# Performance work log

Measured on AMD Instinct MI355X. Metric: run time of the kernel, lower is better.

Reference implementation:

```python
import jax, jax.numpy as jnp
import numpy as np

B, T, D, H = 16, 64, 256, 1536  # batch, num_seq (trg_len), input_dim, hid_dim


def setup_inputs() -> dict:
    key = jax.random.key(0)
    ks = jax.random.split(key, 6)
    def w(k, shape, fan):
        return jax.random.normal(k, shape, jnp.float32) / np.sqrt(fan).astype(np.float32)
    return {
        "batch": jax.random.normal(ks[0], (B, T, D), jnp.float32),
        # PyTorch LSTM params, gate order (i, f, g, o), layer 0 and layer 1
        "W_ih0": w(ks[1], (4 * H, D), H),
        "W_hh0": w(ks[2], (4 * H, H), H),
        "b_ih0": jnp.zeros((4 * H,), jnp.float32),
        "b_hh0": jnp.zeros((4 * H,), jnp.float32),
        "W_ih1": w(ks[3], (4 * H, H), H),
        "W_hh1": w(ks[4], (4 * H, H), H),
        "b_ih1": jnp.zeros((4 * H,), jnp.float32),
        "b_hh1": jnp.zeros((4 * H,), jnp.float32),
    }


def _lstm_cell(pre, c):
    # pre: [4H] pre-activation gates in PyTorch order i, f, g, o
    i, f, g, o = jnp.split(pre, 4, axis=-1)
    c_new = jax.nn.sigmoid(f) * c + jax.nn.sigmoid(i) * jnp.tanh(g)
    h_new = jax.nn.sigmoid(o) * jnp.tanh(c_new)
    return h_new, c_new


def reference(batch, W_ih0, W_hh0, b_ih0, b_hh0, W_ih1, W_hh1, b_ih1, b_hh1):
    hdim = W_hh0.shape[1]
    dt = batch.dtype
    # The original loop runs the unbatched 2-layer LSTM over batch[:, ei, :]
    # (length-B sequence) for ei = 1..T-1, carrying state => one scan over a
    # flattened sequence of length (T-1)*B, ordered ei-major, b-minor.
    seq = batch[:, 1:, :].transpose(1, 0, 2).reshape(-1, batch.shape[2])  # [(T-1)*B, D]
    # Precompute layer-0 input projection as one GEMM (dropout=0.3 is between
    # layers in train mode only; reference is eval mode, so no dropout).
    x_pre0 = seq @ W_ih0.T + (b_ih0 + b_hh0)  # [(T-1)*B, 4H]
    b1 = b_ih1 + b_hh1

    def step(carry, xp0):
        h, c = carry  # each [2, H] (num_layers, hid_dim), unbatched
        h0, c0 = _lstm_cell(xp0 + h[0] @ W_hh0.T, c[0])
        h1, c1 = _lstm_cell(h0 @ W_ih1.T + h[1] @ W_hh1.T + b1, c[1])
        return (jnp.stack([h0, h1]), jnp.stack([c0, c1])), None

    init = (jnp.zeros((2, hdim), dt), jnp.zeros((2, hdim), dt))
    (h_final, c_final), _ = jax.lax.scan(step, init, x_pre0)
    return h_final, c_final  # each [2, H], matching (encoder_hidden, encoder_cell)
```

## Files before the change

### kernel.cpp

```cpp
#include <hip/hip_runtime.h>
#include <cstdint>

#define HDIM   1536
#define DIN    256
#define NSTEP  1008
#define NWG    256
#define TPB    512
#define UPW    6
#define XN     256
#define NREP   8

#define C_H0      0
#define C_H1      1024
#define REP_STRIDE 2048
#define WS_FLAG_W 32768

typedef uint32_t u32x4 __attribute__((ext_vector_type(4)));

__device__ __forceinline__ float bflo(uint32_t p){ union{uint32_t u; float f;} v; v.u = p << 16; return v.f; }
__device__ __forceinline__ float bfhi(uint32_t p){ union{uint32_t u; float f;} v; v.u = p & 0xffff0000u; return v.f; }
__device__ __forceinline__ float bf2f(uint16_t b){ union{uint32_t u; float f;} v; v.u = ((uint32_t)b) << 16; return v.f; }
__device__ __forceinline__ uint16_t f2bf(float f){
    union{float f; uint32_t u;} v; v.f = f;
    uint32_t r = v.u + 0x7fffu + ((v.u >> 16) & 1u);
    return (uint16_t)(r >> 16);
}
__device__ __forceinline__ uint32_t packbf(float lo, float hi){
    return (uint32_t)f2bf(lo) | ((uint32_t)f2bf(hi) << 16);
}
__device__ __forceinline__ float tanh_fast(float x){
    return 1.f - 2.f/(__expf(2.f*x) + 1.f);
}

#if __has_builtin(__builtin_amdgcn_fdot2_f32_bf16)
typedef __bf16 bf16x2 __attribute__((ext_vector_type(2)));
__device__ __forceinline__ float dot2bf(uint32_t a, uint32_t b, float c){
    return __builtin_amdgcn_fdot2_f32_bf16(__builtin_bit_cast(bf16x2, a),
                                           __builtin_bit_cast(bf16x2, b), c, false);
}
#else
__device__ __forceinline__ float dot2bf(uint32_t a, uint32_t b, float c){
    c = fmaf(bflo(a), bflo(b), c);
    c = fmaf(bfhi(a), bfhi(b), c);
    return c;
}
#endif

__device__ __forceinline__ u32x4 poll16(const uint64_t* p){
    u32x4 r;
    asm volatile("global_load_dwordx4 %0, %1, off sc0 sc1\n\t"
                 "s_waitcnt vmcnt(0)"
                 : "=v"(r) : "v"(p) : "memory");
    return r;
}

__device__ __forceinline__ float wave_sum(float x){
    #pragma unroll
    for (int o = 1; o < 64; o <<= 1) x += __shfl_xor(x, o, 64);
    return x;
}

__global__ void init_ws(const uint32_t* __restrict__ w, uint32_t* __restrict__ ws){
    uint64_t* ws64 = (uint64_t*)ws;
    const int i = blockIdx.x * blockDim.x + threadIdx.x;
    if (i < NREP*512){
        const int rep = i >> 9, j = i & 511;
        uint64_t* base = ws64 + rep*REP_STRIDE;
        base[C_H0 + 512 + j] = 0ull;
        base[C_H1 + j]       = 0ull;
        base[C_H1 + 512 + j] = ((uint64_t)1 << 48);
    }
    if (blockIdx.x == 0 && threadIdx.x < 64){
        const int t = threadIdx.x;
        int cnt = 0;
        #pragma unroll
        for (int j = 0; j < 4; ++j){
            const uint32_t v = w[t*4 + j];
            const uint32_t e = (v >> 7) & 0xFFu;
            if (e == 0u || (e >= 0x70u && e <= 0x7Cu)) cnt++;
        }
        #pragma unroll
        for (int o = 1; o < 64; o <<= 1) cnt += __shfl_xor(cnt, o, 64);
        if (t == 0)
            ws[WS_FLAG_W] = (cnt < 128) ? 1u : 0u;
    }
}

__global__ __launch_bounds__(TPB, 2)
void lstm_seq_kernel(const void* __restrict__ batch_,
                     const void* __restrict__ Wih0_,
                     const void* __restrict__ Whh0_,
                     const void* __restrict__ bih0_,
                     const void* __restrict__ bhh0_,
                     const void* __restrict__ Wih1_,
                     const void* __restrict__ Whh1_,
                     const void* __restrict__ bih1_,
                     const void* __restrict__ bhh1_,
                     void* __restrict__ out_,
                     uint32_t* __restrict__ ws)
{
    __shared__ uint32_t lds_w[8*3*8*64];
    __shared__ uint32_t lds_h[1536];
    __shared__ float    lds_pre[48];
    __shared__ float    lds_b[48];
    __shared__ float    lds_c[12];
    __shared__ float    lds_hout[12];

    const int g   = blockIdx.x;
    const int tid = threadIdx.x;
    const int w   = tid >> 6;
    const int l   = tid & 63;

    const uint32_t fp32in = __hip_atomic_load(&ws[WS_FLAG_W],
                             __ATOMIC_RELAXED, __HIP_MEMORY_SCOPE_AGENT);
    uint64_t* ws64 = (uint64_t*)ws;

    if (tid < 24){
        const int uu = tid >> 2, gate = tid & 3;
        const int grow = gate*HDIM + g*UPW + uu;
        if (fp32in){
            lds_b[tid]      = ((const float*)bih0_)[grow] + ((const float*)bhh0_)[grow];
            lds_b[24 + tid] = ((const float*)bih1_)[grow] + ((const float*)bhh1_)[grow];
        } else {
            lds_b[tid]      = bf2f(((const uint16_t*)bih0_)[grow]) + bf2f(((const uint16_t*)bhh0_)[grow]);
            lds_b[24 + tid] = bf2f(((const uint16_t*)bih1_)[grow]) + bf2f(((const uint16_t*)bhh1_)[grow]);
        }
    }
    if (tid < 12){ lds_c[tid] = 0.f; lds_hout[tid] = 0.f; }

    uint32_t w0[3][14];
    uint32_t w1r[3][16];

    if (fp32in){
        const float2* Wih0f = (const float2*)Wih0_;
        const float2* Whh0f = (const float2*)Whh0_;
        const float2* Wih1f = (const float2*)Wih1_;
        const float2* Whh1f = (const float2*)Whh1_;
        #pragma unroll
        for (int j = 0; j < 3; ++j){
            const int rr = w*3 + j;
            const int grow = (rr & 3)*HDIM + g*UPW + (rr >> 2);
            float2 t;
            t = Wih0f[grow*(DIN/2) + l];        w0[j][0] = packbf(t.x, t.y);
            t = Wih0f[grow*(DIN/2) + 64 + l];   w0[j][1] = packbf(t.x, t.y);
            #pragma unroll
            for (int c = 2; c < 14; ++c){
                t = Whh0f[grow*(HDIM/2) + (c-2)*64 + l]; w0[j][c] = packbf(t.x, t.y);
            }
            #pragma unroll
            for (int c = 0; c < 8; ++c){
                t = Wih1f[grow*(HDIM/2) + c*64 + l];
                lds_w[((w*3 + j)*8 + c)*64 + l] = packbf(t.x, t.y);
            }
            #pragma unroll
            for (int c = 8; c < 12; ++c){
                t = Wih1f[grow*(HDIM/2) + c*64 + l]; w1r[j][c-8] = packbf(t.x, t.y);
            }
            #pragma unroll
            for (int c = 12; c < 24; ++c){
                t = Whh1f[grow*(HDIM/2) + (c-12)*64 + l]; w1r[j][c-8] = packbf(t.x, t.y);
            }
        }
    } else {
        const uint32_t* Wih0p = (const uint32_t*)Wih0_;
        const uint32_t* Whh0p = (const uint32_t*)Whh0_;
        const uint32_t* Wih1p = (const uint32_t*)Wih1_;
        const uint32_t* Whh1p = (const uint32_t*)Whh1_;
        #pragma unroll
        for (int j = 0; j < 3; ++j){
            const int rr = w*3 + j;
            const int grow = (rr & 3)*HDIM + g*UPW + (rr >> 2);
            w0[j][0] = Wih0p[grow*(DIN/2) + l];
            w0[j][1] = Wih0p[grow*(DIN/2) + 64 + l];
            #pragma unroll
            for (int c = 2; c < 14; ++c)
                w0[j][c] = Whh0p[grow*(HDIM/2) + (c-2)*64 + l];
            #pragma unroll
            for (int c = 0; c < 8; ++c)
                lds_w[((w*3 + j)*8 + c)*64 + l] = Wih1p[grow*(HDIM/2) + c*64 + l];
            #pragma unroll
            for (int c = 8; c < 12; ++c)
                w1r[j][c-8] = Wih1p[grow*(HDIM/2) + c*64 + l];
            #pragma unroll
            for (int c = 12; c < 24; ++c)
                w1r[j][c-8] = Whh1p[grow*(HDIM/2) + (c-12)*64 + l];
        }
    }

    const int players = tid >> 8;
    const int pidx    = tid & 255;
    uint64_t* myrep   = ws64 + (g & (NREP-1))*REP_STRIDE;

    for (int n = 0; n <= NSTEP; ++n){
        uint32_t xp0, xp1;
        {
            const int nn = (n < NSTEP) ? n : 0;
            const int xbase = ((nn & 15)*64 + (nn >> 4) + 1) * XN;
            if (fp32in){
                const float2* bp = (const float2*)((const float*)batch_ + xbase);
                const float2 t0 = bp[l];
                const float2 t1 = bp[64 + l];
                xp0 = packbf(t0.x, t0.y); xp1 = packbf(t1.x, t1.y);
            } else {
                const uint32_t* bp = (const uint32_t*)batch_ + (xbase >> 1);
                xp0 = bp[l]; xp1 = bp[64 + l];
            }
        }

        u32x4 r;
        {
            const uint64_t* ap = myrep
                + (players ? (C_H1 + (n & 1)*512) : (C_H0 + ((n+1) & 1)*512))
                + 2*pidx;
            const uint32_t want = (uint32_t)n & 0xFFFFu;
            r = poll16(ap);
            while ((r.y >> 16) != want || (r.w >> 16) != want){
                __builtin_amdgcn_s_sleep(1);
                r = poll16(ap);
            }
        }
        {
            const int base = players*768 + 3*pidx;
            lds_h[base]     = r.x;
            lds_h[base + 1] = (r.y & 0xFFFFu) | (r.z << 16);
            lds_h[base + 2] = (r.z >> 16)     | (r.w << 16);
        }
        __syncthreads();

        uint32_t h0p[12], h1p[12];
        #pragma unroll
        for (int k = 0; k < 12; ++k) h0p[k] = lds_h[k*64 + l];
        #pragma unroll
        for (int k = 0; k < 12; ++k) h1p[k] = lds_h[768 + k*64 + l];

        float acc0[3], acc1[3];
        #pragma unroll
        for (int j = 0; j < 3; ++j){
            float a = dot2bf(w0[j][0], xp0, 0.f);
            a = dot2bf(w0[j][1], xp1, a);
            #pragma unroll
            for (int k = 0; k < 12; ++k)
                a = dot2bf(w0[j][k+2], h0p[k], a);
            acc0[j] = a;
        }
        #pragma unroll
        for (int j = 0; j < 3; ++j){
            float a = 0.f;
            #pragma unroll
            for (int k = 0; k < 8; ++k)
                a = dot2bf(lds_w[((w*3 + j)*8 + k)*64 + l], h0p[k], a);
            #pragma unroll
            for (int k = 8; k < 12; ++k)
                a = dot2bf(w1r[j][k-8], h0p[k], a);
            #pragma unroll
            for (int k = 0; k < 12; ++k)
                a = dot2bf(w1r[j][k+4], h1p[k], a);
            acc1[j] = a;
        }
        #pragma unroll
        for (int j = 0; j < 3; ++j){
            const float r0 = wave_sum(acc0[j]);
            const float r1 = wave_sum(acc1[j]);
            if (l == 0){
                lds_pre[w*3 + j]      = r0;
                lds_pre[24 + w*3 + j] = r1;
            }
        }
        __syncthreads();

        if (w == 0){
            float hpub = 0.f;
            if (l < 12){
                const int layer = l / 6, uu = l % 6;
                const bool active = (layer == 0) ? (n < NSTEP) : (n >= 1);
                if (active){
                    const float* pre = &lds_pre[layer*24 + uu*4];
                    const float* bb  = &lds_b[layer*24 + uu*4];
                    const float gi = pre[0] + bb[0];
                    const float gf = pre[1] + bb[1];
                    const float gg = pre[2] + bb[2];
                    const float go = pre[3] + bb[3];
                    const float si = 1.f/(1.f + __expf(-gi));
                    const float sf = 1.f/(1.f + __expf(-gf));
                    const float so = 1.f/(1.f + __expf(-go));
                    const float cn = sf*lds_c[l] + si*tanh_fast(gg);
                    const float hn = so * tanh_fast(cn);
                    lds_c[l] = cn;
                    lds_hout[l] = hn;
                    hpub = hn;
                }
            }
            const int slot = l & 3;
            const int b3 = 3*slot;
            const float s0 = __shfl(hpub, b3,     64);
            const float s1 = __shfl(hpub, b3 + 1, 64);
            const float s2 = __shfl(hpub, b3 + 2, 64);
            if (l < 4*NREP && n < NSTEP){
                const bool isL1 = (slot >= 2);
                if (!isL1 || n >= 1){
                    const uint64_t tag = (uint64_t)((uint32_t)(n + 1) & 0xFFFFu);
                    const uint64_t pk = (uint64_t)f2bf(s0)
                                      | ((uint64_t)f2bf(s1) << 16)
                                      | ((uint64_t)f2bf(s2) << 32)
                                      | (tag << 48);
                    uint64_t* dst = ws64 + (l >> 2)*REP_STRIDE
                        + (isL1 ? (C_H1 + ((n+1) & 1)*512 + 2*g + (slot - 2))
                                : (C_H0 + (n & 1)*512 + 2*g + slot));
                    __hip_atomic_store(dst, pk, __ATOMIC_RELAXED, __HIP_MEMORY_SCOPE_AGENT);
                }
            }
        }
    }

    if (tid < 12){
        const int layer = tid / 6, uu = tid % 6;
        const int oi = layer*HDIM + g*UPW + uu;
        if (fp32in){
            ((float*)out_)[oi]        = lds_hout[tid];
            ((float*)out_)[3072 + oi] = lds_c[tid];
        } else {
            ((uint16_t*)out_)[oi]        = f2bf(lds_hout[tid]);
            ((uint16_t*)out_)[3072 + oi] = f2bf(lds_c[tid]);
        }
    }
}

extern "C" void kernel_launch(void* const* d_in, const int* in_sizes, int n_in,
                              void* d_out, int out_size, void* d_ws, size_t ws_size,
                              hipStream_t stream)
{
    (void)in_sizes; (void)n_in; (void)out_size; (void)ws_size;
    const void* batch = d_in[0];
    const void* Wih0  = d_in[1];
    const void* Whh0  = d_in[2];
    const void* bih0  = d_in[3];
    const void* bhh0  = d_in[4];
    const void* Wih1  = d_in[5];
    const void* Whh1  = d_in[6];
    const void* bih1  = d_in[7];
    const void* bhh1  = d_in[8];
    void* out = d_out;
    uint32_t* ws = (uint32_t*)d_ws;

    hipLaunchKernelGGL(init_ws, dim3((NREP*512 + 255)/256), dim3(256), 0, stream,
                       (const uint32_t*)Whh0, ws);

    void* args[] = { &batch, &Wih0, &Whh0, &bih0, &bhh0,
                     &Wih1, &Whh1, &bih1, &bhh1, &out, &ws };
    hipLaunchCooperativeKernel((const void*)lstm_seq_kernel,
                               dim3(NWG), dim3(TPB), args, 0, stream);
}
```

Measured before the change: 3.493 ms.

## Give each wave one hidden unit, poll per-unit tagged slots, decouple layers

Reorganises the persistent cooperative LSTM so each of 6 waves owns one hidden unit with all four gate rows in registers. Gate math and state stay in-wave, which removes the LDS pre-activation exchange and both block-wide barriers per step. Hidden states are now published as per-unit 32-bit tagged words and polled with 12 loads per lane. Layer-0 work can proceed while wave 1 polls layer-1 state, synchronised through LDS flags. The trade-off is more polling traffic per step and higher register pressure from fewer threads per block.

```diff
diff --git a/kernel.cpp b/kernel.cpp
--- a/kernel.cpp
+++ b/kernel.cpp
@@ -5,17 +5,15 @@
 #define DIN    256
 #define NSTEP  1008
 #define NWG    256
-#define TPB    512
+#define TPB    384
 #define UPW    6
-#define XN     256
 #define NREP   8
 
-#define C_H0      0
-#define C_H1      1024
-#define REP_STRIDE 2048
-#define WS_FLAG_W 32768
-
-typedef uint32_t u32x4 __attribute__((ext_vector_type(4)));
+#define REP_W     6144
+#define H1_OFF    3072
+#define WS_FLAG_W (NREP*REP_W)
+
+typedef uint32_t u32x2 __attribute__((ext_vector_type(2)));
 
 __device__ __forceinline__ float bflo(uint32_t p){ union{uint32_t u; float f;} v; v.u = p << 16; return v.f; }
 __device__ __forceinline__ float bfhi(uint32_t p){ union{uint32_t u; float f;} v; v.u = p & 0xffff0000u; return v.f; }
@@ -46,29 +44,76 @@
 }
 #endif
 
-__device__ __forceinline__ u32x4 poll16(const uint64_t* p){
-    u32x4 r;
-    asm volatile("global_load_dwordx4 %0, %1, off sc0 sc1\n\t"
-                 "s_waitcnt vmcnt(0)"
-                 : "=v"(r) : "v"(p) : "memory");
-    return r;
-}
-
 __device__ __forceinline__ float wave_sum(float x){
     #pragma unroll
     for (int o = 1; o < 64; o <<= 1) x += __shfl_xor(x, o, 64);
     return x;
 }
 
+template<int SLOW>
+__device__ __forceinline__ void poll12(const char* a, uint32_t want, uint32_t pr[12]){
+    u32x2 q0,q1,q2,q3,q4,q5,q6,q7,q8,q9,qa,qb;
+    const uint32_t want2 = want | (want << 16);
+    int t = 0;
+    for (;;){
+        asm volatile(
+            "global_load_dwordx2 %0,  %12, off offset:-2816 sc0 sc1\n\t"
+            "global_load_dwordx2 %1,  %12, off offset:-2304 sc0 sc1\n\t"
+            "global_load_dwordx2 %2,  %12, off offset:-1792 sc0 sc1\n\t"
+            "global_load_dwordx2 %3,  %12, off offset:-1280 sc0 sc1\n\t"
+            "global_load_dwordx2 %4,  %12, off offset:-768 sc0 sc1\n\t"
+            "global_load_dwordx2 %5,  %12, off offset:-256 sc0 sc1\n\t"
+            "global_load_dwordx2 %6,  %12, off offset:256 sc0 sc1\n\t"
+            "global_load_dwordx2 %7,  %12, off offset:768 sc0 sc1\n\t"
+            "global_load_dwordx2 %8,  %12, off offset:1280 sc0 sc1\n\t"
+            "global_load_dwordx2 %9,  %12, off offset:1792 sc0 sc1\n\t"
+            "global_load_dwordx2 %10, %12, off offset:2304 sc0 sc1\n\t"
+            "global_load_dwordx2 %11, %12, off offset:2816 sc0 sc1\n\t"
+            "s_waitcnt vmcnt(0)"
+            : "=v"(q0),"=v"(q1),"=v"(q2),"=v"(q3),"=v"(q4),"=v"(q5),
+              "=v"(q6),"=v"(q7),"=v"(q8),"=v"(q9),"=v"(qa),"=v"(qb)
+            : "v"(a) : "memory");
+        uint32_t d;
+        d  = __builtin_amdgcn_perm(q0.y, q0.x, 0x07060302u) ^ want2;
+        d |= __builtin_amdgcn_perm(q1.y, q1.x, 0x07060302u) ^ want2;
+        d |= __builtin_amdgcn_perm(q2.y, q2.x, 0x07060302u) ^ want2;
+        d |= __builtin_amdgcn_perm(q3.y, q3.x, 0x07060302u) ^ want2;
+        d |= __builtin_amdgcn_perm(q4.y, q4.x, 0x07060302u) ^ want2;
+        d |= __builtin_amdgcn_perm(q5.y, q5.x, 0x07060302u) ^ want2;
+        d |= __builtin_amdgcn_perm(q6.y, q6.x, 0x07060302u) ^ want2;
+        d |= __builtin_amdgcn_perm(q7.y, q7.x, 0x07060302u) ^ want2;
+        d |= __builtin_amdgcn_perm(q8.y, q8.x, 0x07060302u) ^ want2;
+        d |= __builtin_amdgcn_perm(q9.y, q9.x, 0x07060302u) ^ want2;
+        d |= __builtin_amdgcn_perm(qa.y, qa.x, 0x07060302u) ^ want2;
+        d |= __builtin_amdgcn_perm(qb.y, qb.x, 0x07060302u) ^ want2;
+        if (__all(d == 0u)) break;
+        if (SLOW){
+            if (t == 0) __builtin_amdgcn_s_sleep(8);
+            else        __builtin_amdgcn_s_sleep(2);
+        } else {
+            __builtin_amdgcn_s_sleep(2);
+        }
+        ++t;
+    }
+    pr[0]  = __builtin_amdgcn_perm(q0.y, q0.x, 0x05040100u);
+    pr[1]  = __builtin_amdgcn_perm(q1.y, q1.x, 0x05040100u);
+    pr[2]  = __builtin_amdgcn_perm(q2.y, q2.x, 0x05040100u);
+    pr[3]  = __builtin_amdgcn_perm(q3.y, q3.x, 0x05040100u);
+    pr[4]  = __builtin_amdgcn_perm(q4.y, q4.x, 0x05040100u);
+    pr[5]  = __builtin_amdgcn_perm(q5.y, q5.x, 0x05040100u);
+    pr[6]  = __builtin_amdgcn_perm(q6.y, q6.x, 0x05040100u);
+    pr[7]  = __builtin_amdgcn_perm(q7.y, q7.x, 0x05040100u);
+    pr[8]  = __builtin_amdgcn_perm(q8.y, q8.x, 0x05040100u);
+    pr[9]  = __builtin_amdgcn_perm(q9.y, q9.x, 0x05040100u);
+    pr[10] = __builtin_amdgcn_perm(qa.y, qa.x, 0x05040100u);
+    pr[11] = __builtin_amdgcn_perm(qb.y, qb.x, 0x05040100u);
+}
+
 __global__ void init_ws(const uint32_t* __restrict__ w, uint32_t* __restrict__ ws){
-    uint64_t* ws64 = (uint64_t*)ws;
     const int i = blockIdx.x * blockDim.x + threadIdx.x;
-    if (i < NREP*512){
-        const int rep = i >> 9, j = i & 511;
-        uint64_t* base = ws64 + rep*REP_STRIDE;
-        base[C_H0 + 512 + j] = 0ull;
-        base[C_H1 + j]       = 0ull;
-        base[C_H1 + 512 + j] = ((uint64_t)1 << 48);
+    if (i < NREP*REP_W){
+        const int j = i % REP_W;
+        ws[i] = (j >= H1_OFF + 1536) ? 0x00010000u : 0u;
     }
     if (blockIdx.x == 0 && threadIdx.x < 64){
         const int t = threadIdx.x;
@@ -86,7 +131,7 @@
     }
 }
 
-__global__ __launch_bounds__(TPB, 2)
+__global__ __launch_bounds__(TPB, 1)
 void lstm_seq_kernel(const void* __restrict__ batch_,
                      const void* __restrict__ Wih0_,
                      const void* __restrict__ Whh0_,
@@ -99,37 +144,25 @@
                      void* __restrict__ out_,
                      uint32_t* __restrict__ ws)
 {
-    __shared__ uint32_t lds_w[8*3*8*64];
-    __shared__ uint32_t lds_h[1536];
-    __shared__ float    lds_pre[48];
-    __shared__ float    lds_b[48];
-    __shared__ float    lds_c[12];
-    __shared__ float    lds_hout[12];
+    __shared__ uint32_t lds_w[UPW*4*8*64];
+    __shared__ uint32_t lds_h0[768];
+    __shared__ uint32_t lds_h1[768];
+    __shared__ int      lds_flag[2];
 
     const int g   = blockIdx.x;
     const int tid = threadIdx.x;
     const int w   = tid >> 6;
     const int l   = tid & 63;
+    const int U   = g*UPW + w;
 
     const uint32_t fp32in = __hip_atomic_load(&ws[WS_FLAG_W],
                              __ATOMIC_RELAXED, __HIP_MEMORY_SCOPE_AGENT);
-    uint64_t* ws64 = (uint64_t*)ws;
-
-    if (tid < 24){
-        const int uu = tid >> 2, gate = tid & 3;
-        const int grow = gate*HDIM + g*UPW + uu;
-        if (fp32in){
-            lds_b[tid]      = ((const float*)bih0_)[grow] + ((const float*)bhh0_)[grow];
-            lds_b[24 + tid] = ((const float*)bih1_)[grow] + ((const float*)bhh1_)[grow];
-        } else {
-            lds_b[tid]      = bf2f(((const uint16_t*)bih0_)[grow]) + bf2f(((const uint16_t*)bhh0_)[grow]);
-            lds_b[24 + tid] = bf2f(((const uint16_t*)bih1_)[grow]) + bf2f(((const uint16_t*)bhh1_)[grow]);
-        }
-    }
-    if (tid < 12){ lds_c[tid] = 0.f; lds_hout[tid] = 0.f; }
-
-    uint32_t w0[3][14];
-    uint32_t w1r[3][16];
+
+    if (tid < 2) lds_flag[tid] = -1;
+
+    uint32_t w0[4][14];
+    uint32_t w1[4][16];
+    float bb0[4], bb1[4];
 
     if (fp32in){
         const float2* Wih0f = (const float2*)Wih0_;
@@ -137,29 +170,30 @@
         const float2* Wih1f = (const float2*)Wih1_;
         const float2* Whh1f = (const float2*)Whh1_;
         #pragma unroll
-        for (int j = 0; j < 3; ++j){
-            const int rr = w*3 + j;
-            const int grow = (rr & 3)*HDIM + g*UPW + (rr >> 2);
+        for (int r = 0; r < 4; ++r){
+            const int grow = r*HDIM + U;
             float2 t;
-            t = Wih0f[grow*(DIN/2) + l];        w0[j][0] = packbf(t.x, t.y);
-            t = Wih0f[grow*(DIN/2) + 64 + l];   w0[j][1] = packbf(t.x, t.y);
-            #pragma unroll
-            for (int c = 2; c < 14; ++c){
-                t = Whh0f[grow*(HDIM/2) + (c-2)*64 + l]; w0[j][c] = packbf(t.x, t.y);
+            t = Wih0f[grow*(DIN/2) + l];      w0[r][0] = packbf(t.x, t.y);
+            t = Wih0f[grow*(DIN/2) + 64 + l]; w0[r][1] = packbf(t.x, t.y);
+            #pragma unroll
+            for (int c = 0; c < 12; ++c){
+                t = Whh0f[grow*(HDIM/2) + c*64 + l]; w0[r][c+2] = packbf(t.x, t.y);
             }
             #pragma unroll
             for (int c = 0; c < 8; ++c){
                 t = Wih1f[grow*(HDIM/2) + c*64 + l];
-                lds_w[((w*3 + j)*8 + c)*64 + l] = packbf(t.x, t.y);
+                lds_w[(w*4 + r)*512 + c*64 + l] = packbf(t.x, t.y);
             }
             #pragma unroll
             for (int c = 8; c < 12; ++c){
-                t = Wih1f[grow*(HDIM/2) + c*64 + l]; w1r[j][c-8] = packbf(t.x, t.y);
-            }
-            #pragma unroll
-            for (int c = 12; c < 24; ++c){
-                t = Whh1f[grow*(HDIM/2) + (c-12)*64 + l]; w1r[j][c-8] = packbf(t.x, t.y);
-            }
+                t = Wih1f[grow*(HDIM/2) + c*64 + l]; w1[r][c-8] = packbf(t.x, t.y);
+            }
+            #pragma unroll
+            for (int c = 0; c < 12; ++c){
+                t = Whh1f[grow*(HDIM/2) + c*64 + l]; w1[r][c+4] = packbf(t.x, t.y);
+            }
+            bb0[r] = ((const float*)bih0_)[grow] + ((const float*)bhh0_)[grow];
+            bb1[r] = ((const float*)bih1_)[grow] + ((const float*)bhh1_)[grow];
         }
     } else {
         const uint32_t* Wih0p = (const uint32_t*)Wih0_;
@@ -167,35 +201,32 @@
         const uint32_t* Wih1p = (const uint32_t*)Wih1_;
         const uint32_t* Whh1p = (const uint32_t*)Whh1_;
         #pragma unroll
-        for (int j = 0; j < 3; ++j){
-            const int rr = w*3 + j;
-            const int grow = (rr & 3)*HDIM + g*UPW + (rr >> 2);
-            w0[j][0] = Wih0p[grow*(DIN/2) + l];
-            w0[j][1] = Wih0p[grow*(DIN/2) + 64 + l];
-            #pragma unroll
-            for (int c = 2; c < 14; ++c)
-                w0[j][c] = Whh0p[grow*(HDIM/2) + (c-2)*64 + l];
+        for (int r = 0; r < 4; ++r){
+            const int grow = r*HDIM + U;
+            w0[r][0] = Wih0p[grow*(DIN/2) + l];
+            w0[r][1] = Wih0p[grow*(DIN/2) + 64 + l];
+            #pragma unroll
+            for (int c = 0; c < 12; ++c) w0[r][c+2] = Whh0p[grow*(HDIM/2) + c*64 + l];
             #pragma unroll
             for (int c = 0; c < 8; ++c)
-                lds_w[((w*3 + j)*8 + c)*64 + l] = Wih1p[grow*(HDIM/2) + c*64 + l];
-            #pragma unroll
-            for (int c = 8; c < 12; ++c)
-                w1r[j][c-8] = Wih1p[grow*(HDIM/2) + c*64 + l];
-            #pragma unroll
-            for (int c = 12; c < 24; ++c)
-                w1r[j][c-8] = Whh1p[grow*(HDIM/2) + (c-12)*64 + l];
-        }
-    }
-
-    const int players = tid >> 8;
-    const int pidx    = tid & 255;
-    uint64_t* myrep   = ws64 + (g & (NREP-1))*REP_STRIDE;
+                lds_w[(w*4 + r)*512 + c*64 + l] = Wih1p[grow*(HDIM/2) + c*64 + l];
+            #pragma unroll
+            for (int c = 8; c < 12; ++c) w1[r][c-8] = Wih1p[grow*(HDIM/2) + c*64 + l];
+            #pragma unroll
+            for (int c = 0; c < 12; ++c) w1[r][c+4] = Whh1p[grow*(HDIM/2) + c*64 + l];
+            bb0[r] = bf2f(((const uint16_t*)bih0_)[grow]) + bf2f(((const uint16_t*)bhh0_)[grow]);
+            bb1[r] = bf2f(((const uint16_t*)bih1_)[grow]) + bf2f(((const uint16_t*)bhh1_)[grow]);
+        }
+    }
+    __syncthreads();
+
+    float c0 = 0.f, c1 = 0.f, h0f = 0.f, h1f = 0.f;
+    uint32_t* wsrep = ws + (g & (NREP-1))*REP_W;
 
     for (int n = 0; n <= NSTEP; ++n){
-        uint32_t xp0, xp1;
-        {
-            const int nn = (n < NSTEP) ? n : 0;
-            const int xbase = ((nn & 15)*64 + (nn >> 4) + 1) * XN;
+        uint32_t xp0 = 0, xp1 = 0;
+        if (n < NSTEP){
+            const int xbase = ((n & 15)*64 + (n >> 4) + 1) * DIN;
             if (fp32in){
                 const float2* bp = (const float2*)((const float*)batch_ + xbase);
                 const float2 t0 = bp[l];
@@ -207,120 +238,112 @@
             }
         }
 
-        u32x4 r;
-        {
-            const uint64_t* ap = myrep
-                + (players ? (C_H1 + (n & 1)*512) : (C_H0 + ((n+1) & 1)*512))
-                + 2*pidx;
-            const uint32_t want = (uint32_t)n & 0xFFFFu;
-            r = poll16(ap);
-            while ((r.y >> 16) != want || (r.w >> 16) != want){
+        uint32_t h0p[12];
+        uint32_t h1p[12];
+
+        if (w == 1 && n >= 1){
+            const char* a = (const char*)(wsrep + H1_OFF + (n & 1)*1536) + 8*l + 2816;
+            poll12<0>(a, (uint32_t)n, h1p);
+            #pragma unroll
+            for (int k = 0; k < 12; ++k) lds_h1[k*64 + l] = h1p[k];
+            __hip_atomic_store(&lds_flag[1], n, __ATOMIC_RELEASE, __HIP_MEMORY_SCOPE_WORKGROUP);
+        }
+
+        if (w == 0){
+            const char* a = (const char*)(wsrep + ((n+1) & 1)*1536) + 8*l + 2816;
+            poll12<1>(a, (uint32_t)n, h0p);
+            #pragma unroll
+            for (int k = 0; k < 12; ++k) lds_h0[k*64 + l] = h0p[k];
+            __hip_atomic_store(&lds_flag[0], n, __ATOMIC_RELEASE, __HIP_MEMORY_SCOPE_WORKGROUP);
+        } else {
+            while (__hip_atomic_load(&lds_flag[0], __ATOMIC_ACQUIRE, __HIP_MEMORY_SCOPE_WORKGROUP) < n)
                 __builtin_amdgcn_s_sleep(1);
-                r = poll16(ap);
-            }
-        }
-        {
-            const int base = players*768 + 3*pidx;
-            lds_h[base]     = r.x;
-            lds_h[base + 1] = (r.y & 0xFFFFu) | (r.z << 16);
-            lds_h[base + 2] = (r.z >> 16)     | (r.w << 16);
-        }
-        __syncthreads();
-
-        uint32_t h0p[12], h1p[12];
-        #pragma unroll
-        for (int k = 0; k < 12; ++k) h0p[k] = lds_h[k*64 + l];
-        #pragma unroll
-        for (int k = 0; k < 12; ++k) h1p[k] = lds_h[768 + k*64 + l];
-
-        float acc0[3], acc1[3];
-        #pragma unroll
-        for (int j = 0; j < 3; ++j){
-            float a = dot2bf(w0[j][0], xp0, 0.f);
-            a = dot2bf(w0[j][1], xp1, a);
-            #pragma unroll
-            for (int k = 0; k < 12; ++k)
-                a = dot2bf(w0[j][k+2], h0p[k], a);
-            acc0[j] = a;
-        }
-        #pragma unroll
-        for (int j = 0; j < 3; ++j){
-            float a = 0.f;
-            #pragma unroll
-            for (int k = 0; k < 8; ++k)
-                a = dot2bf(lds_w[((w*3 + j)*8 + k)*64 + l], h0p[k], a);
-            #pragma unroll
-            for (int k = 8; k < 12; ++k)
-                a = dot2bf(w1r[j][k-8], h0p[k], a);
-            #pragma unroll
-            for (int k = 0; k < 12; ++k)
-                a = dot2bf(w1r[j][k+4], h1p[k], a);
-            acc1[j] = a;
-        }
-        #pragma unroll
-        for (int j = 0; j < 3; ++j){
-            const float r0 = wave_sum(acc0[j]);
-            const float r1 = wave_sum(acc1[j]);
-            if (l == 0){
-                lds_pre[w*3 + j]      = r0;
-                lds_pre[24 + w*3 + j] = r1;
-            }
-        }
-        __syncthreads();
-
-        if (w == 0){
-            float hpub = 0.f;
-            if (l < 12){
-                const int layer = l / 6, uu = l % 6;
-                const bool active = (layer == 0) ? (n < NSTEP) : (n >= 1);
-                if (active){
-                    const float* pre = &lds_pre[layer*24 + uu*4];
-                    const float* bb  = &lds_b[layer*24 + uu*4];
-                    const float gi = pre[0] + bb[0];
-                    const float gf = pre[1] + bb[1];
-                    const float gg = pre[2] + bb[2];
-                    const float go = pre[3] + bb[3];
-                    const float si = 1.f/(1.f + __expf(-gi));
-                    const float sf = 1.f/(1.f + __expf(-gf));
-                    const float so = 1.f/(1.f + __expf(-go));
-                    const float cn = sf*lds_c[l] + si*tanh_fast(gg);
-                    const float hn = so * tanh_fast(cn);
-                    lds_c[l] = cn;
-                    lds_hout[l] = hn;
-                    hpub = hn;
-                }
-            }
-            const int slot = l & 3;
-            const int b3 = 3*slot;
-            const float s0 = __shfl(hpub, b3,     64);
-            const float s1 = __shfl(hpub, b3 + 1, 64);
-            const float s2 = __shfl(hpub, b3 + 2, 64);
-            if (l < 4*NREP && n < NSTEP){
-                const bool isL1 = (slot >= 2);
-                if (!isL1 || n >= 1){
-                    const uint64_t tag = (uint64_t)((uint32_t)(n + 1) & 0xFFFFu);
-                    const uint64_t pk = (uint64_t)f2bf(s0)
-                                      | ((uint64_t)f2bf(s1) << 16)
-                                      | ((uint64_t)f2bf(s2) << 32)
-                                      | (tag << 48);
-                    uint64_t* dst = ws64 + (l >> 2)*REP_STRIDE
-                        + (isL1 ? (C_H1 + ((n+1) & 1)*512 + 2*g + (slot - 2))
-                                : (C_H0 + (n & 1)*512 + 2*g + slot));
-                    __hip_atomic_store(dst, pk, __ATOMIC_RELAXED, __HIP_MEMORY_SCOPE_AGENT);
-                }
-            }
-        }
-    }
-
-    if (tid < 12){
-        const int layer = tid / 6, uu = tid % 6;
-        const int oi = layer*HDIM + g*UPW + uu;
+            #pragma unroll
+            for (int k = 0; k < 12; ++k) h0p[k] = lds_h0[k*64 + l];
+        }
+
+        if (n < NSTEP){
+            __builtin_amdgcn_s_setprio(1);
+            float acc[4];
+            #pragma unroll
+            for (int r = 0; r < 4; ++r){
+                float a = dot2bf(w0[r][0], xp0, 0.f);
+                a = dot2bf(w0[r][1], xp1, a);
+                #pragma unroll
+                for (int k = 0; k < 12; ++k) a = dot2bf(w0[r][k+2], h0p[k], a);
+                acc[r] = a;
+            }
+            #pragma unroll
+            for (int r = 0; r < 4; ++r) acc[r] = wave_sum(acc[r]);
+            const float gi = acc[0] + bb0[0];
+            const float gf = acc[1] + bb0[1];
+            const float gg = acc[2] + bb0[2];
+            const float go = acc[3] + bb0[3];
+            const float si = 1.f/(1.f + __expf(-gi));
+            const float sf = 1.f/(1.f + __expf(-gf));
+            const float so = 1.f/(1.f + __expf(-go));
+            c0  = sf*c0 + si*tanh_fast(gg);
+            h0f = so*tanh_fast(c0);
+            const uint32_t pk = (uint32_t)f2bf(h0f) | ((uint32_t)(n + 1) << 16);
+            if (l < NREP)
+                __hip_atomic_store(ws + l*REP_W + (n & 1)*1536 + U, pk,
+                                   __ATOMIC_RELAXED, __HIP_MEMORY_SCOPE_AGENT);
+            __builtin_amdgcn_s_setprio(0);
+        }
+
+        if (n >= 1){
+            if (w != 1){
+                while (__hip_atomic_load(&lds_flag[1], __ATOMIC_ACQUIRE, __HIP_MEMORY_SCOPE_WORKGROUP) < n)
+                    __builtin_amdgcn_s_sleep(1);
+                #pragma unroll
+                for (int k = 0; k < 12; ++k) h1p[k] = lds_h1[k*64 + l];
+            }
+            float acc[4];
+            #pragma unroll
+            for (int r = 0; r < 4; ++r){
+                float a = 0.f;
+                #pragma unroll
+                for (int c = 0; c < 8; ++c)
+                    a = dot2bf(lds_w[(w*4 + r)*512 + c*64 + l], h0p[c], a);
+                #pragma unroll
+                for (int c = 8; c < 12; ++c) a = dot2bf(w1[r][c-8], h0p[c], a);
+                #pragma unroll
+                for (int k = 0; k < 12; ++k) a = dot2bf(w1[r][k+4], h1p[k], a);
+                acc[r] = a;
+            }
+            #pragma unroll
+            for (int r = 0; r < 4; ++r) acc[r] = wave_sum(acc[r]);
+            const float gi = acc[0] + bb1[0];
+            const float gf = acc[1] + bb1[1];
+            const float gg = acc[2] + bb1[2];
+            const float go = acc[3] + bb1[3];
+            const float si = 1.f/(1.f + __expf(-gi));
+            const float sf = 1.f/(1.f + __expf(-gf));
+            const float so = 1.f/(1.f + __expf(-go));
+            c1  = sf*c1 + si*tanh_fast(gg);
+            h1f = so*tanh_fast(c1);
+            if (n < NSTEP){
+                const uint32_t pk = (uint32_t)f2bf(h1f) | ((uint32_t)(n + 1) << 16);
+                if (l < NREP)
+                    __hip_atomic_store(ws + l*REP_W + H1_OFF + ((n+1) & 1)*1536 + U, pk,
+                                       __ATOMIC_RELAXED, __HIP_MEMORY_SCOPE_AGENT);
+            }
+        }
+    }
+
+    if (l == 0){
         if (fp32in){
-            ((float*)out_)[oi]        = lds_hout[tid];
-            ((float*)out_)[3072 + oi] = lds_c[tid];
+            float* o = (float*)out_;
+            o[U]               = h0f;
+            o[HDIM + U]        = h1f;
+            o[3072 + U]        = c0;
+            o[3072 + HDIM + U] = c1;
         } else {
-            ((uint16_t*)out_)[oi]        = f2bf(lds_hout[tid]);
-            ((uint16_t*)out_)[3072 + oi] = f2bf(lds_c[tid]);
+            uint16_t* o = (uint16_t*)out_;
+            o[U]               = f2bf(h0f);
+            o[HDIM + U]        = f2bf(h1f);
+            o[3072 + U]        = f2bf(c0);
+            o[3072 + HDIM + U] = f2bf(c1);
         }
     }
 }
@@ -342,7 +365,7 @@
     void* out = d_out;
     uint32_t* ws = (uint32_t*)d_ws;
 
-    hipLaunchKernelGGL(init_ws, dim3((NREP*512 + 255)/256), dim3(256), 0, stream,
+    hipLaunchKernelGGL(init_ws, dim3((NREP*REP_W + 255)/256), dim3(256), 0, stream,
                        (const uint32_t*)Whh0, ws);
 
     void* args[] = { &batch, &Wih0, &Whh0, &bih0, &bhh0,
```

Result: no change. 3.452 ms (median of 2 runs) (-1.2%).
